# Kernel tuning notes

Measured on AMD Instinct MI355X. Metric: run time of the kernel, lower is better.

Reference implementation:

```python
import jax, jax.numpy as jnp
import numpy as np

B, S, D, H = 2, 2048, 1024, 16
HD = D // H
NEG = -10000000000.0

def setup_inputs() -> dict:
    key = jax.random.key(0)
    ks = jax.random.split(key, 9)
    s = 1.0 / np.sqrt(D)
    return {
        "x": jax.random.normal(ks[0], (B, S, D), dtype=jnp.float32),
        "Wq": jax.random.uniform(ks[1], (D, D), jnp.float32, -s, s),
        "bq": jax.random.uniform(ks[2], (D,), jnp.float32, -s, s),
        "Wk": jax.random.uniform(ks[3], (D, D), jnp.float32, -s, s),
        "bk": jax.random.uniform(ks[4], (D,), jnp.float32, -s, s),
        "Wv": jax.random.uniform(ks[5], (D, D), jnp.float32, -s, s),
        "bv": jax.random.uniform(ks[6], (D,), jnp.float32, -s, s),
        "Wo": jax.random.uniform(ks[7], (D, D), jnp.float32, -s, s),
        "bo": jax.random.uniform(ks[8], (D,), jnp.float32, -s, s),
    }

def reference(x, Wq, bq, Wk, bk, Wv, bv, Wo, bo):
    b, s, _ = x.shape
    def split_heads(t):
        return t.reshape(b, s, H, HD).transpose(0, 2, 1, 3)  # [b,h,s,hd]
    Q = split_heads(x @ Wq + bq)
    K = split_heads(x @ Wk + bk)
    V = split_heads(x @ Wv + bv)
    scores = jnp.einsum('bhqd,bhkd->bhqk', Q, K) / jnp.sqrt(jnp.float32(HD))
    causal = jnp.tril(jnp.ones((s, s), dtype=bool))
    scores = jnp.where(causal[None, None], scores, NEG)
    attn = jax.nn.softmax(scores, axis=-1)
    ctx = jnp.einsum('bhqk,bhkd->bhqd', attn, V)
    ctx = ctx.transpose(0, 2, 1, 3).reshape(b, s, D)
    return ctx @ Wo + bo
```

## Files before the change

kernel.cpp:

```cpp
#include <hip/hip_runtime.h>
#include <hip/hip_bf16.h>

#define BB 2
#define SS 2048
#define DD 1024
#define HH 16
#define HD 64
#define MM (BB*SS)

typedef __attribute__((ext_vector_type(8))) short bf16x8;
typedef __attribute__((ext_vector_type(4))) float f32x4;

#define QSCALE 0.18033688f

static __device__ __forceinline__ unsigned short f2bf(float f) {
    unsigned int u = __builtin_bit_cast(unsigned int, f);
    u += 0x7fffu + ((u >> 16) & 1u);
    return (unsigned short)(u >> 16);
}

static __device__ __forceinline__ void gload16(const unsigned short* g, unsigned short* l) {
    __builtin_amdgcn_global_load_lds(
        (const __attribute__((address_space(1))) unsigned int*)g,
        (__attribute__((address_space(3))) unsigned int*)l, 16, 0, 0);
}

__global__ __launch_bounds__(256) void convert_x_bf16(const float* __restrict__ x,
                                                      unsigned short* __restrict__ xb)
{
    const size_t i = ((size_t)blockIdx.x * 256 + threadIdx.x) * 8;
    float4 a = *(const float4*)(x + i);
    float4 b = *(const float4*)(x + i + 4);
    union { unsigned short u[8]; bf16x8 v; } pk;
    pk.u[0] = f2bf(a.x); pk.u[1] = f2bf(a.y); pk.u[2] = f2bf(a.z); pk.u[3] = f2bf(a.w);
    pk.u[4] = f2bf(b.x); pk.u[5] = f2bf(b.y); pk.u[6] = f2bf(b.z); pk.u[7] = f2bf(b.w);
    *(bf16x8*)(xb + i) = pk.v;
}

__global__ __launch_bounds__(256) void transpose_w_bf16(const float* __restrict__ W0,
                                                        const float* __restrict__ W1,
                                                        const float* __restrict__ W2,
                                                        const float* __restrict__ W3,
                                                        unsigned short* __restrict__ Wt)
{
    __shared__ unsigned short Ts[64][72];
    const int t = threadIdx.x;
    const float* W = blockIdx.z == 0 ? W0 : blockIdx.z == 1 ? W1 : blockIdx.z == 2 ? W2 : W3;
    unsigned short* out = Wt + (size_t)blockIdx.z * DD * DD;
    const int n0 = blockIdx.x * 64, k0 = blockIdx.y * 64;
#pragma unroll
    for (int i = 0; i < 4; ++i) {
        const int r = (t >> 4) + i * 16;
        const int c = (t & 15) * 4;
        float4 v = *(const float4*)(W + (size_t)(k0 + r) * DD + n0 + c);
        Ts[c + 0][r] = f2bf(v.x); Ts[c + 1][r] = f2bf(v.y);
        Ts[c + 2][r] = f2bf(v.z); Ts[c + 3][r] = f2bf(v.w);
    }
    __syncthreads();
#pragma unroll
    for (int j = 0; j < 2; ++j) {
        const int ch = j * 256 + t;
        const int rn = ch >> 3, ck = (ch & 7) * 8;
        bf16x8 v = *(const bf16x8*)&Ts[rn][ck];
        *(bf16x8*)(out + (size_t)(n0 + rn) * DD + k0 + ck) = v;
    }
}

__global__ __launch_bounds__(256) void gemm_mfma(const unsigned short* __restrict__ A,
                                                 const unsigned short* __restrict__ Bt,
                                                 const float* __restrict__ bias0,
                                                 const float* __restrict__ bias1,
                                                 const float* __restrict__ bias2,
                                                 unsigned short* __restrict__ Qb,
                                                 unsigned short* __restrict__ Kb,
                                                 unsigned short* __restrict__ Vb,
                                                 float* __restrict__ outf,
                                                 int mode)
{
    __shared__ unsigned short As[128 * 32];
    __shared__ unsigned short Bs[128 * 32];

    const int t = threadIdx.x;
    const int w = t >> 6, l = t & 63;
    const int lane16 = l & 15, quad = l >> 4;
    const int m0 = blockIdx.x * 128, n0 = blockIdx.y * 128;
    const int wm = (w & 1) * 64, wn = (w >> 1) * 64;

    f32x4 acc[4][4] = {};

    const int c0 = t, c1 = 256 + t;
    const int r0 = c0 >> 2, kc0 = (c0 & 3) * 8;
    const int r1 = c1 >> 2, kc1 = (c1 & 3) * 8;

    for (int k0 = 0; k0 < DD; k0 += 32) {
        __syncthreads();
        gload16(A  + (size_t)(m0 + r0) * DD + k0 + kc0, As + c0 * 8);
        gload16(A  + (size_t)(m0 + r1) * DD + k0 + kc1, As + c1 * 8);
        gload16(Bt + (size_t)(n0 + r0) * DD + k0 + kc0, Bs + c0 * 8);
        gload16(Bt + (size_t)(n0 + r1) * DD + k0 + kc1, Bs + c1 * 8);
        __syncthreads();

        bf16x8 af[4], bfr[4];
#pragma unroll
        for (int mt = 0; mt < 4; ++mt)
            af[mt] = *(const bf16x8*)&As[(wm + mt * 16 + lane16) * 32 + quad * 8];
#pragma unroll
        for (int nt = 0; nt < 4; ++nt)
            bfr[nt] = *(const bf16x8*)&Bs[(wn + nt * 16 + lane16) * 32 + quad * 8];
#pragma unroll
        for (int mt = 0; mt < 4; ++mt)
#pragma unroll
            for (int nt = 0; nt < 4; ++nt)
                acc[mt][nt] = __builtin_amdgcn_mfma_f32_16x16x32_bf16(af[mt], bfr[nt], acc[mt][nt], 0, 0, 0);
    }

    if (mode == 0) {
        const int which = n0 >> 10;
        const float* bias = which == 0 ? bias0 : which == 1 ? bias1 : bias2;
#pragma unroll
        for (int nt = 0; nt < 4; ++nt) {
            const int gcol = n0 + wn + nt * 16 + lane16;
            const int cd = gcol & 1023;
            const float bv = bias[cd];
            const int h_ = cd >> 6, d = cd & 63;
            if (which == 2) {
#pragma unroll
                for (int mt = 0; mt < 4; ++mt) {
                    const int row0 = m0 + wm + mt * 16 + quad * 4;
                    const int b_ = row0 >> 11, s0 = row0 & 2047;
                    union { unsigned short u[4]; uint2 v; } pk;
#pragma unroll
                    for (int r = 0; r < 4; ++r) pk.u[r] = f2bf(acc[mt][nt][r] + bv);
                    *(uint2*)(Vb + ((size_t)(b_ * HH + h_) * HD + d) * SS + s0) = pk.v;
                }
            } else {
                unsigned short* dst3 = which == 0 ? Qb : Kb;
                const float sc_ = which == 0 ? QSCALE : 1.0f;
#pragma unroll
                for (int mt = 0; mt < 4; ++mt)
#pragma unroll
                    for (int r = 0; r < 4; ++r) {
                        const int row = m0 + wm + mt * 16 + quad * 4 + r;
                        const int b_ = row >> 11, s_ = row & 2047;
                        dst3[(((size_t)(b_ * HH + h_) * SS + s_) * HD) + d] =
                            f2bf((acc[mt][nt][r] + bv) * sc_);
                    }
            }
        }
    } else {
#pragma unroll
        for (int nt = 0; nt < 4; ++nt) {
            const int gcol = n0 + wn + nt * 16 + lane16;
            const float bv = bias0[gcol];
#pragma unroll
            for (int mt = 0; mt < 4; ++mt)
#pragma unroll
                for (int r = 0; r < 4; ++r) {
                    const int row = m0 + wm + mt * 16 + quad * 4 + r;
                    outf[(size_t)row * DD + gcol] = acc[mt][nt][r] + bv;
                }
        }
    }
}

__global__ __launch_bounds__(512) void attn_mfma(const unsigned short* __restrict__ Q,
                                                 const unsigned short* __restrict__ K,
                                                 const unsigned short* __restrict__ V,
                                                 unsigned short* __restrict__ ctx)
{
    __shared__ unsigned short Ks[2][4096];
    __shared__ unsigned short Vs[2][4096];
    __shared__ unsigned short Ps[8][1280];

    const int t = threadIdx.x;
    const int w = t >> 6, l = t & 63;
    const int lane16 = l & 15, quad = l >> 4;
    const int bid = blockIdx.x;
    const int qblk = (SS / 128 - 1) - (bid >> 5);
    const int hb = bid & 31;
    const int h = hb & 15, b = hb >> 4;
    const int q0 = qblk * 128;
    const size_t bh = (size_t)(b * HH + h) * SS;
    const unsigned short* Vg = V + (size_t)(b * HH + h) * HD * SS;

    const int wrow0 = q0 + w * 16;
    bf16x8 qf0 = *(const bf16x8*)(Q + (bh + wrow0 + lane16) * HD + quad * 8);
    bf16x8 qf1 = *(const bf16x8*)(Q + (bh + wrow0 + lane16) * HD + 32 + quad * 8);

    f32x4 Oc[4] = {};
    float lpart[4] = {};

    const int ntiles = 2 * qblk + 2;
    const int skc = t >> 8, sr = (t >> 2) & 63, sj = t & 3;

    {
        gload16(K  + (bh + sr) * HD + skc * 32 + sj * 8, &Ks[0][t * 8]);
        gload16(Vg + (size_t)sr * SS + skc * 32 + sj * 8, &Vs[0][t * 8]);
    }

    for (int kt = 0; kt < ntiles; ++kt) {
        __syncthreads();
        if (kt + 1 < ntiles) {
            const int k1 = (kt + 1) * 64;
            const int bi = (kt + 1) & 1;
            gload16(K  + (bh + k1 + sr) * HD + skc * 32 + sj * 8, &Ks[bi][t * 8]);
            gload16(Vg + (size_t)sr * SS + k1 + skc * 32 + sj * 8, &Vs[bi][t * 8]);
        }
        const int k0 = kt * 64;
        if (k0 > wrow0 + 15) continue;
        const unsigned short* Kb = Ks[kt & 1];
        const unsigned short* Vb = Vs[kt & 1];

        f32x4 sc[4] = {};
#pragma unroll
        for (int nt = 0; nt < 4; ++nt) {
            bf16x8 k0f = *(const bf16x8*)&Kb[(nt * 16 + lane16) * 32 + quad * 8];
            bf16x8 k1f = *(const bf16x8*)&Kb[2048 + (nt * 16 + lane16) * 32 + quad * 8];
            sc[nt] = __builtin_amdgcn_mfma_f32_16x16x32_bf16(qf0, k0f, sc[nt], 0, 0, 0);
            sc[nt] = __builtin_amdgcn_mfma_f32_16x16x32_bf16(qf1, k1f, sc[nt], 0, 0, 0);
        }

        float pr[4][4];
        if (k0 + 63 > wrow0) {
#pragma unroll
            for (int r = 0; r < 4; ++r) {
                const int row = wrow0 + quad * 4 + r;
#pragma unroll
                for (int nt = 0; nt < 4; ++nt)
                    if (k0 + nt * 16 + lane16 > row) sc[nt][r] = -1e30f;
            }
        }
#pragma unroll
        for (int nt = 0; nt < 4; ++nt)
#pragma unroll
            for (int r = 0; r < 4; ++r) pr[nt][r] = __builtin_amdgcn_exp2f(sc[nt][r]);
#pragma unroll
        for (int r = 0; r < 4; ++r)
            lpart[r] += (pr[0][r] + pr[1][r]) + (pr[2][r] + pr[3][r]);

        unsigned short* Pw = Ps[w];
#pragma unroll
        for (int nt = 0; nt < 4; ++nt) {
            const int plane = (nt >> 1) * 640, colin = (nt & 1) * 16 + lane16;
#pragma unroll
            for (int r = 0; r < 4; ++r)
                Pw[plane + (quad * 4 + r) * 40 + colin] = f2bf(pr[nt][r]);
        }
        bf16x8 pf0 = *(const bf16x8*)&Pw[lane16 * 40 + quad * 8];
        bf16x8 pf1 = *(const bf16x8*)&Pw[640 + lane16 * 40 + quad * 8];

#pragma unroll
        for (int dt = 0; dt < 4; ++dt) {
            bf16x8 v0 = *(const bf16x8*)&Vb[(dt * 16 + lane16) * 32 + quad * 8];
            bf16x8 v1 = *(const bf16x8*)&Vb[2048 + (dt * 16 + lane16) * 32 + quad * 8];
            Oc[dt] = __builtin_amdgcn_mfma_f32_16x16x32_bf16(pf0, v0, Oc[dt], 0, 0, 0);
            Oc[dt] = __builtin_amdgcn_mfma_f32_16x16x32_bf16(pf1, v1, Oc[dt], 0, 0, 0);
        }
    }

#pragma unroll
    for (int off = 1; off < 16; off <<= 1)
#pragma unroll
        for (int r = 0; r < 4; ++r) lpart[r] += __shfl_xor(lpart[r], off);

#pragma unroll
    for (int r = 0; r < 4; ++r) {
        const float inv = 1.f / lpart[r];
        const int row = wrow0 + quad * 4 + r;
        unsigned short* dst = ctx + ((size_t)(b * SS) + row) * DD + h * HD + lane16;
#pragma unroll
        for (int dt = 0; dt < 4; ++dt) dst[dt * 16] = f2bf(Oc[dt][r] * inv);
    }
}

extern "C" void kernel_launch(void* const* d_in, const int* in_sizes, int n_in,
                              void* d_out, int out_size, void* d_ws, size_t ws_size,
                              hipStream_t stream) {
    const float* x  = (const float*)d_in[0];
    const float* Wq = (const float*)d_in[1];
    const float* bq = (const float*)d_in[2];
    const float* Wk = (const float*)d_in[3];
    const float* bk = (const float*)d_in[4];
    const float* Wv = (const float*)d_in[5];
    const float* bv = (const float*)d_in[6];
    const float* Wo = (const float*)d_in[7];
    const float* bo = (const float*)d_in[8];
    float* out = (float*)d_out;

    unsigned short* xb  = (unsigned short*)d_ws;
    unsigned short* Wt  = xb  + (size_t)MM * DD;
    unsigned short* Qb  = Wt  + (size_t)4 * DD * DD;
    unsigned short* Kb  = Qb  + (size_t)MM * DD;
    unsigned short* Vb  = Kb  + (size_t)MM * DD;
    unsigned short* ctxb = Vb + (size_t)MM * DD;

    convert_x_bf16<<<(MM * DD) / (8 * 256), 256, 0, stream>>>(x, xb);
    transpose_w_bf16<<<dim3(16, 16, 4), 256, 0, stream>>>(Wq, Wk, Wv, Wo, Wt);

    gemm_mfma<<<dim3(MM / 128, 3072 / 128), 256, 0, stream>>>(
        xb, Wt, bq, bk, bv, Qb, Kb, Vb, nullptr, 0);

    attn_mfma<<<(SS / 128) * HH * BB, 512, 0, stream>>>(Qb, Kb, Vb, ctxb);

    gemm_mfma<<<dim3(MM / 128, DD / 128), 256, 0, stream>>>(
        ctxb, Wt + (size_t)3 * DD * DD, bo, nullptr, nullptr,
        nullptr, nullptr, nullptr, out, 1);
}
```

Before: 206.9 us.

## Swizzle LDS layouts, widen GEMM K-tile, merge prep kernels, rebalance attention blocks

Merges the x conversion and weight transpose into one prep kernel, saving a launch. Doubles the GEMM K-step to 64 and stores the A/B tiles in an XOR-swizzled LDS layout to cut bank conflicts and halve the number of barriers. Applies the same swizzle to the K/V tiles in attention. It also reorders the attention block index so the second half of the grid runs small query blocks first, which changes how causal work is spread across the grid. The larger LDS tiles may lower occupancy.

```diff
diff --git a/kernel.cpp b/kernel.cpp
--- a/kernel.cpp
+++ b/kernel.cpp
@@ -25,29 +25,32 @@
         (__attribute__((address_space(3))) unsigned int*)l, 16, 0, 0);
 }
 
-__global__ __launch_bounds__(256) void convert_x_bf16(const float* __restrict__ x,
-                                                      unsigned short* __restrict__ xb)
+__global__ __launch_bounds__(256) void prep_kernel(const float* __restrict__ x,
+                                                   const float* __restrict__ W0,
+                                                   const float* __restrict__ W1,
+                                                   const float* __restrict__ W2,
+                                                   const float* __restrict__ W3,
+                                                   unsigned short* __restrict__ xb,
+                                                   unsigned short* __restrict__ Wt)
 {
-    const size_t i = ((size_t)blockIdx.x * 256 + threadIdx.x) * 8;
-    float4 a = *(const float4*)(x + i);
-    float4 b = *(const float4*)(x + i + 4);
-    union { unsigned short u[8]; bf16x8 v; } pk;
-    pk.u[0] = f2bf(a.x); pk.u[1] = f2bf(a.y); pk.u[2] = f2bf(a.z); pk.u[3] = f2bf(a.w);
-    pk.u[4] = f2bf(b.x); pk.u[5] = f2bf(b.y); pk.u[6] = f2bf(b.z); pk.u[7] = f2bf(b.w);
-    *(bf16x8*)(xb + i) = pk.v;
-}
-
-__global__ __launch_bounds__(256) void transpose_w_bf16(const float* __restrict__ W0,
-                                                        const float* __restrict__ W1,
-                                                        const float* __restrict__ W2,
-                                                        const float* __restrict__ W3,
-                                                        unsigned short* __restrict__ Wt)
-{
+    const int t = threadIdx.x;
+    const int bid = blockIdx.x;
+    if (bid < 2048) {
+        const size_t i = ((size_t)bid * 256 + t) * 8;
+        float4 a = *(const float4*)(x + i);
+        float4 b = *(const float4*)(x + i + 4);
+        union { unsigned short u[8]; bf16x8 v; } pk;
+        pk.u[0] = f2bf(a.x); pk.u[1] = f2bf(a.y); pk.u[2] = f2bf(a.z); pk.u[3] = f2bf(a.w);
+        pk.u[4] = f2bf(b.x); pk.u[5] = f2bf(b.y); pk.u[6] = f2bf(b.z); pk.u[7] = f2bf(b.w);
+        *(bf16x8*)(xb + i) = pk.v;
+        return;
+    }
     __shared__ unsigned short Ts[64][72];
-    const int t = threadIdx.x;
-    const float* W = blockIdx.z == 0 ? W0 : blockIdx.z == 1 ? W1 : blockIdx.z == 2 ? W2 : W3;
-    unsigned short* out = Wt + (size_t)blockIdx.z * DD * DD;
-    const int n0 = blockIdx.x * 64, k0 = blockIdx.y * 64;
+    const int wsel = (bid - 2048) >> 8;
+    const int rem  = (bid - 2048) & 255;
+    const float* W = wsel == 0 ? W0 : wsel == 1 ? W1 : wsel == 2 ? W2 : W3;
+    unsigned short* out = Wt + (size_t)wsel * DD * DD;
+    const int n0 = (rem & 15) * 64, k0 = (rem >> 4) * 64;
 #pragma unroll
     for (int i = 0; i < 4; ++i) {
         const int r = (t >> 4) + i * 16;
@@ -77,8 +80,8 @@
                                                  float* __restrict__ outf,
                                                  int mode)
 {
-    __shared__ unsigned short As[128 * 32];
-    __shared__ unsigned short Bs[128 * 32];
+    __shared__ unsigned short As[128 * 64];
+    __shared__ unsigned short Bs[128 * 64];
 
     const int t = threadIdx.x;
     const int w = t >> 6, l = t & 63;
@@ -88,30 +91,43 @@
 
     f32x4 acc[4][4] = {};
 
-    const int c0 = t, c1 = 256 + t;
-    const int r0 = c0 >> 2, kc0 = (c0 & 3) * 8;
-    const int r1 = c1 >> 2, kc1 = (c1 & 3) * 8;
-
-    for (int k0 = 0; k0 < DD; k0 += 32) {
+    int srow[4], skcg[4];
+#pragma unroll
+    for (int j = 0; j < 4; ++j) {
+        const int c = t + j * 256;
+        srow[j] = c >> 3;
+        skcg[j] = (c & 7) ^ (srow[j] & 7);
+    }
+
+    for (int k0 = 0; k0 < DD; k0 += 64) {
         __syncthreads();
-        gload16(A  + (size_t)(m0 + r0) * DD + k0 + kc0, As + c0 * 8);
-        gload16(A  + (size_t)(m0 + r1) * DD + k0 + kc1, As + c1 * 8);
-        gload16(Bt + (size_t)(n0 + r0) * DD + k0 + kc0, Bs + c0 * 8);
-        gload16(Bt + (size_t)(n0 + r1) * DD + k0 + kc1, Bs + c1 * 8);
+#pragma unroll
+        for (int j = 0; j < 4; ++j) {
+            const int c = t + j * 256;
+            gload16(A  + (size_t)(m0 + srow[j]) * DD + k0 + skcg[j] * 8, As + c * 8);
+            gload16(Bt + (size_t)(n0 + srow[j]) * DD + k0 + skcg[j] * 8, Bs + c * 8);
+        }
         __syncthreads();
 
-        bf16x8 af[4], bfr[4];
-#pragma unroll
-        for (int mt = 0; mt < 4; ++mt)
-            af[mt] = *(const bf16x8*)&As[(wm + mt * 16 + lane16) * 32 + quad * 8];
-#pragma unroll
-        for (int nt = 0; nt < 4; ++nt)
-            bfr[nt] = *(const bf16x8*)&Bs[(wn + nt * 16 + lane16) * 32 + quad * 8];
-#pragma unroll
-        for (int mt = 0; mt < 4; ++mt)
-#pragma unroll
-            for (int nt = 0; nt < 4; ++nt)
-                acc[mt][nt] = __builtin_amdgcn_mfma_f32_16x16x32_bf16(af[mt], bfr[nt], acc[mt][nt], 0, 0, 0);
+#pragma unroll
+        for (int h = 0; h < 2; ++h) {
+            bf16x8 af[4], bfr[4];
+#pragma unroll
+            for (int mt = 0; mt < 4; ++mt) {
+                const int row = wm + mt * 16 + lane16;
+                af[mt] = *(const bf16x8*)&As[(row * 8 + ((h * 4 + quad) ^ (row & 7))) * 8];
+            }
+#pragma unroll
+            for (int nt = 0; nt < 4; ++nt) {
+                const int row = wn + nt * 16 + lane16;
+                bfr[nt] = *(const bf16x8*)&Bs[(row * 8 + ((h * 4 + quad) ^ (row & 7))) * 8];
+            }
+#pragma unroll
+            for (int mt = 0; mt < 4; ++mt)
+#pragma unroll
+                for (int nt = 0; nt < 4; ++nt)
+                    acc[mt][nt] = __builtin_amdgcn_mfma_f32_16x16x32_bf16(af[mt], bfr[nt], acc[mt][nt], 0, 0, 0);
+        }
     }
 
     if (mode == 0) {
@@ -176,8 +192,10 @@
     const int w = t >> 6, l = t & 63;
     const int lane16 = l & 15, quad = l >> 4;
     const int bid = blockIdx.x;
-    const int qblk = (SS / 128 - 1) - (bid >> 5);
-    const int hb = bid & 31;
+    const int halfg = bid >> 8, idx = bid & 255;
+    const int qb_ = idx >> 5;
+    const int qblk = halfg ? qb_ : 15 - qb_;
+    const int hb = idx & 31;
     const int h = hb & 15, b = hb >> 4;
     const int q0 = qblk * 128;
     const size_t bh = (size_t)(b * HH + h) * SS;
@@ -191,11 +209,12 @@
     float lpart[4] = {};
 
     const int ntiles = 2 * qblk + 2;
-    const int skc = t >> 8, sr = (t >> 2) & 63, sj = t & 3;
+    const int sr = t >> 3;
+    const int sg = (t & 7) ^ (sr & 7);
 
     {
-        gload16(K  + (bh + sr) * HD + skc * 32 + sj * 8, &Ks[0][t * 8]);
-        gload16(Vg + (size_t)sr * SS + skc * 32 + sj * 8, &Vs[0][t * 8]);
+        gload16(K  + (bh + sr) * HD + sg * 8, &Ks[0][t * 8]);
+        gload16(Vg + (size_t)sr * SS + sg * 8, &Vs[0][t * 8]);
     }
 
     for (int kt = 0; kt < ntiles; ++kt) {
@@ -203,19 +222,20 @@
         if (kt + 1 < ntiles) {
             const int k1 = (kt + 1) * 64;
             const int bi = (kt + 1) & 1;
-            gload16(K  + (bh + k1 + sr) * HD + skc * 32 + sj * 8, &Ks[bi][t * 8]);
-            gload16(Vg + (size_t)sr * SS + k1 + skc * 32 + sj * 8, &Vs[bi][t * 8]);
+            gload16(K  + (bh + k1 + sr) * HD + sg * 8, &Ks[bi][t * 8]);
+            gload16(Vg + (size_t)sr * SS + k1 + sg * 8, &Vs[bi][t * 8]);
         }
         const int k0 = kt * 64;
         if (k0 > wrow0 + 15) continue;
-        const unsigned short* Kb = Ks[kt & 1];
-        const unsigned short* Vb = Vs[kt & 1];
+        const unsigned short* Kt = Ks[kt & 1];
+        const unsigned short* Vt = Vs[kt & 1];
 
         f32x4 sc[4] = {};
 #pragma unroll
         for (int nt = 0; nt < 4; ++nt) {
-            bf16x8 k0f = *(const bf16x8*)&Kb[(nt * 16 + lane16) * 32 + quad * 8];
-            bf16x8 k1f = *(const bf16x8*)&Kb[2048 + (nt * 16 + lane16) * 32 + quad * 8];
+            const int row = nt * 16 + lane16;
+            bf16x8 k0f = *(const bf16x8*)&Kt[(row * 8 + (quad ^ (row & 7))) * 8];
+            bf16x8 k1f = *(const bf16x8*)&Kt[(row * 8 + ((4 + quad) ^ (row & 7))) * 8];
             sc[nt] = __builtin_amdgcn_mfma_f32_16x16x32_bf16(qf0, k0f, sc[nt], 0, 0, 0);
             sc[nt] = __builtin_amdgcn_mfma_f32_16x16x32_bf16(qf1, k1f, sc[nt], 0, 0, 0);
         }
@@ -251,8 +271,9 @@
 
 #pragma unroll
         for (int dt = 0; dt < 4; ++dt) {
-            bf16x8 v0 = *(const bf16x8*)&Vb[(dt * 16 + lane16) * 32 + quad * 8];
-            bf16x8 v1 = *(const bf16x8*)&Vb[2048 + (dt * 16 + lane16) * 32 + quad * 8];
+            const int drow = dt * 16 + lane16;
+            bf16x8 v0 = *(const bf16x8*)&Vt[(drow * 8 + (quad ^ (drow & 7))) * 8];
+            bf16x8 v1 = *(const bf16x8*)&Vt[(drow * 8 + ((4 + quad) ^ (drow & 7))) * 8];
             Oc[dt] = __builtin_amdgcn_mfma_f32_16x16x32_bf16(pf0, v0, Oc[dt], 0, 0, 0);
             Oc[dt] = __builtin_amdgcn_mfma_f32_16x16x32_bf16(pf1, v1, Oc[dt], 0, 0, 0);
         }
@@ -294,8 +315,7 @@
     unsigned short* Vb  = Kb  + (size_t)MM * DD;
     unsigned short* ctxb = Vb + (size_t)MM * DD;
 
-    convert_x_bf16<<<(MM * DD) / (8 * 256), 256, 0, stream>>>(x, xb);
-    transpose_w_bf16<<<dim3(16, 16, 4), 256, 0, stream>>>(Wq, Wk, Wv, Wo, Wt);
+    prep_kernel<<<2048 + 1024, 256, 0, stream>>>(x, Wq, Wk, Wv, Wo, xb, Wt);
 
     gemm_mfma<<<dim3(MM / 128, 3072 / 128), 256, 0, stream>>>(
         xb, Wt, bq, bk, bv, Qb, Kb, Vb, nullptr, 0);
```

Measured after the change: 197.7 us. 1.05x faster.
